# Optimization experiments

Measured on AMD Instinct MI355X. Metric: run time of the kernel, lower is better.

## Reference

```python
import jax, jax.numpy as jnp
import numpy as np

# config constants
B, L, ENC_IN = 8, 512, 7
D_MODEL = 768
EXPAND = 2
D_INNER = D_MODEL * EXPAND          # 1536
DT_RANK = (D_MODEL + 15) // 16      # 48
N_STATE = 16                         # configs.d_ff acts as SSM state size
K_CONV = 4
E_LAYERS = 2
C_OUT = 7
PRED_LEN = 96
EPS = 1e-5


def rmsnorm(x, w):
    return x * jax.lax.rsqrt(jnp.mean(x * x, axis=-1, keepdims=True) + EPS) * w


def silu(x):
    return x * jax.nn.sigmoid(x)


def positional_embedding(l, d):
    pos = np.arange(l, dtype=np.float32)[:, None]
    div = np.exp(np.arange(0, d, 2, dtype=np.float32) * (-np.log(10000.0) / d))
    pe = np.zeros((l, d), dtype=np.float32)
    pe[:, 0::2] = np.sin(pos * div)
    pe[:, 1::2] = np.cos(pos * div)
    return jnp.asarray(pe)


def causal_dwconv(x, w, b):
    # x: [b, d, l], w: [d, 1, k]; torch pads k-1 both sides then slices [:l] == left-pad k-1
    y = jax.lax.conv_general_dilated(
        x, w, window_strides=(1,), padding=[(K_CONV - 1, 0)],
        dimension_numbers=('NCH', 'OIH', 'NCH'), feature_group_count=D_INNER)
    return y + b[None, :, None]


def selective_scan(u, delta, A, Bm, Cm, Dp):
    # u, delta: [b,l,d]; A: [d,n]; Bm, Cm: [b,l,n]; Dp: [d]
    deltaA = jnp.exp(jnp.einsum('bld,dn->bldn', delta, A))          # [b,l,d,n]
    deltaBu = (delta * u)[..., None] * Bm[:, :, None, :]             # [b,l,d,n]

    def step(xc, inp):
        dA, dBu, Ct = inp                                            # [b,d,n],[b,d,n],[b,n]
        xc = dA * xc + dBu
        return xc, jnp.einsum('bdn,bn->bd', xc, Ct)

    b, l, d = u.shape
    x0 = jnp.zeros((b, d, A.shape[1]), u.dtype)
    _, ys = jax.lax.scan(step, x0, (jnp.moveaxis(deltaA, 1, 0),
                                    jnp.moveaxis(deltaBu, 1, 0),
                                    jnp.moveaxis(Cm, 1, 0)))
    y = jnp.moveaxis(ys, 0, 1)                                       # [b,l,d]
    return y + u * Dp


def mamba_block(x, in_w, conv_w, conv_b, xproj_w, dtproj_w, dtproj_b, A_log, Dp, outproj_w):
    xr = x @ in_w.T                                                  # [b,l,2*d_inner]
    xs, res = xr[..., :D_INNER], xr[..., D_INNER:]
    xs = causal_dwconv(jnp.swapaxes(xs, 1, 2), conv_w, conv_b)
    xs = silu(jnp.swapaxes(xs, 1, 2))
    # ssm
    A = -jnp.exp(A_log)
    x_dbl = xs @ xproj_w.T                                           # [b,l,dt_rank+2n]
    delta = x_dbl[..., :DT_RANK]
    Bm = x_dbl[..., DT_RANK:DT_RANK + N_STATE]
    Cm = x_dbl[..., DT_RANK + N_STATE:]
    delta = jax.nn.softplus(delta @ dtproj_w.T + dtproj_b)
    y = selective_scan(xs, delta, A, Bm, Cm, Dp)
    y = y * silu(res)
    return y @ outproj_w.T


def setup_inputs() -> dict:
    key = jax.random.key(0)
    ks = iter(jax.random.split(key, 32))
    s = 0.02
    d = {}
    d['x'] = jax.random.normal(next(ks), (B, L, ENC_IN), jnp.float32)
    d['token_w'] = jax.random.normal(next(ks), (D_MODEL, ENC_IN, 3), jnp.float32) * s
    d['time_w'] = jax.random.normal(next(ks), (D_MODEL, 1), jnp.float32) * s
    d['norm_w'] = jnp.ones((E_LAYERS, D_MODEL), jnp.float32)
    d['in_w'] = jax.random.normal(next(ks), (E_LAYERS, 2 * D_INNER, D_MODEL), jnp.float32) * s
    d['conv_w'] = jax.random.normal(next(ks), (E_LAYERS, D_INNER, 1, K_CONV), jnp.float32) * s
    d['conv_b'] = jnp.zeros((E_LAYERS, D_INNER), jnp.float32)
    d['xproj_w'] = jax.random.normal(next(ks), (E_LAYERS, DT_RANK + 2 * N_STATE, D_INNER), jnp.float32) * s
    d['dtproj_w'] = jax.random.normal(next(ks), (E_LAYERS, D_INNER, DT_RANK), jnp.float32) * s
    d['dtproj_b'] = jnp.zeros((E_LAYERS, D_INNER), jnp.float32)
    A = np.tile(np.arange(1, N_STATE + 1, dtype=np.float32)[None, :], (D_INNER, 1))
    d['A_log'] = jnp.tile(jnp.log(jnp.asarray(A))[None], (E_LAYERS, 1, 1))
    d['Dp'] = jnp.ones((E_LAYERS, D_INNER), jnp.float32)
    d['outproj_w'] = jax.random.normal(next(ks), (E_LAYERS, D_MODEL, D_INNER), jnp.float32) * s
    d['final_norm_w'] = jnp.ones((D_MODEL,), jnp.float32)
    d['out_w'] = jax.random.normal(next(ks), (C_OUT, D_MODEL), jnp.float32) * s
    return d


def reference(x, token_w, time_w, norm_w, in_w, conv_w, conv_b, xproj_w,
              dtproj_w, dtproj_b, A_log, Dp, outproj_w, final_norm_w, out_w):
    # instance normalization (mean/std detached)
    mean_enc = jax.lax.stop_gradient(jnp.mean(x, axis=1, keepdims=True))
    xc = x - mean_enc
    std_enc = jax.lax.stop_gradient(jnp.sqrt(jnp.var(xc, axis=1, keepdims=True) + 1e-5))
    xc = xc / std_enc
    # DataEmbedding: circular conv token emb + sinusoidal pos + timeF linear
    xp = jnp.pad(jnp.swapaxes(xc, 1, 2), ((0, 0), (0, 0), (1, 1)), mode='wrap')
    tok = jax.lax.conv_general_dilated(xp, token_w, (1,), 'VALID',
                                       dimension_numbers=('NCH', 'OIH', 'NCH'))
    tok = jnp.swapaxes(tok, 1, 2)                                    # [b,l,d_model]
    x_mark = (jnp.arange(L, dtype=x.dtype) / L)[None, :, None]       # [1,l,1]
    h = tok + positional_embedding(L, D_MODEL)[None] + x_mark @ time_w.T
    for e in range(E_LAYERS):
        h = mamba_block(rmsnorm(h, norm_w[e]), in_w[e], conv_w[e], conv_b[e],
                        xproj_w[e], dtproj_w[e], dtproj_b[e], A_log[e], Dp[e],
                        outproj_w[e]) + h
    h = rmsnorm(h, final_norm_w)
    out = h @ out_w.T
    out = out * std_enc + mean_enc
    return out[:, -PRED_LEN:, :]
```

## Files before the change

kernel.cpp:

```cpp
#include <hip/hip_runtime.h>
#include <hip/hip_bf16.h>
#include <math.h>

#define BSZ 8
#define LSEQ 512
#define ENC_IN 7
#define D_MODEL 768
#define D_INNER 1536
#define DT_RANK 48
#define N_STATE 16
#define K_CONV 4
#define E_LAYERS 2
#define C_OUT 7
#define PRED_LEN 96
#define EPSV 1e-5f
#define XN 80
#define KSPLIT 4

#define ROWS (BSZ*LSEQ)
#define NC 16
#define CL (LSEQ/NC)
#define NTILE (LSEQ/16)
#define LOG2E 1.44269504088896f

typedef __bf16 bf16x8 __attribute__((ext_vector_type(8)));
typedef float  f32x4  __attribute__((ext_vector_type(4)));

__device__ __forceinline__ float fexp2(float x) {
    float r;
    asm("v_exp_f32 %0, %1" : "=v"(r) : "v"(x));
    return r;
}
__device__ __forceinline__ float softplusf(float v) {
    return fmaxf(v, 0.f) + log1pf(__expf(-fabsf(v)));
}
__device__ __forceinline__ void glds16(const char* g, char* l) {
    __builtin_amdgcn_global_load_lds((const __attribute__((address_space(1))) unsigned int*)g,
                                     (__attribute__((address_space(3))) unsigned int*)l, 16, 0, 0);
}

__device__ __forceinline__ float block_sum(float v, float* tmp) {
    #pragma unroll
    for (int off = 32; off > 0; off >>= 1) v += __shfl_down(v, off);
    int lane = threadIdx.x & 63, wid = threadIdx.x >> 6;
    __syncthreads();
    if (lane == 0) tmp[wid] = v;
    __syncthreads();
    return tmp[0] + tmp[1] + tmp[2] + tmp[3];
}

__global__ __launch_bounds__(256) void cvt_all(const float* __restrict__ in_w,
                                               const float* __restrict__ outw,
                                               const float* __restrict__ xpw,
                                               const float* __restrict__ dtw,
                                               __hip_bfloat16* __restrict__ inw_bf,
                                               __hip_bfloat16* __restrict__ outw_bf,
                                               __hip_bfloat16* __restrict__ xpw_bf,
                                               __hip_bfloat16* __restrict__ dtw_bf) {
    const int N1 = E_LAYERS*2*D_INNER*D_MODEL;
    const int N2 = E_LAYERS*D_MODEL*D_INNER;
    const int N3 = E_LAYERS*XN*D_INNER;
    const int N4 = E_LAYERS*D_INNER*64;
    int i = blockIdx.x*256 + threadIdx.x;
    if (i < N1) {
        inw_bf[i] = __float2bfloat16(in_w[i]);
    } else if (i < N1+N2) {
        int j = i - N1; outw_bf[j] = __float2bfloat16(outw[j]);
    } else if (i < N1+N2+N3) {
        int j = i - N1 - N2; xpw_bf[j] = __float2bfloat16(xpw[j]);
    } else if (i < N1+N2+N3+N4) {
        int j = i - N1 - N2 - N3;
        int r = j >> 6, c = j & 63;
        dtw_bf[j] = __float2bfloat16(c < DT_RANK ? dtw[r*DT_RANK + c] : 0.f);
    }
}

__global__ __launch_bounds__(256) void stats_kernel(const float* __restrict__ x,
                                                    float* __restrict__ mean,
                                                    float* __restrict__ stdv) {
    int bc = blockIdx.x;
    int b = bc / ENC_IN, c = bc % ENC_IN;
    __shared__ float tmp[4];
    float s = 0.f, sq = 0.f;
    for (int l = threadIdx.x; l < LSEQ; l += 256) {
        float v = x[((size_t)(b*LSEQ + l))*ENC_IN + c];
        s += v; sq += v*v;
    }
    s = block_sum(s, tmp);
    sq = block_sum(sq, tmp);
    if (threadIdx.x == 0) {
        float m = s / LSEQ;
        float var = sq / LSEQ - m*m;
        if (var < 0.f) var = 0.f;
        mean[bc] = m;
        stdv[bc] = sqrtf(var + EPSV);
    }
}

__global__ __launch_bounds__(256) void embed_kernel(const float* __restrict__ x,
                                                    const float* __restrict__ token_w,
                                                    const float* __restrict__ time_w,
                                                    const float* __restrict__ mean,
                                                    const float* __restrict__ stdv,
                                                    float* __restrict__ h) {
    int bl = blockIdx.x;
    int b = bl >> 9, l = bl & 511;
    __shared__ float sxc[ENC_IN*3];
    if (threadIdx.x < ENC_IN*3) {
        int c = threadIdx.x / 3, k = threadIdx.x % 3;
        int lk = (l + k - 1) & 511;
        float v = x[((size_t)(b*LSEQ + lk))*ENC_IN + c];
        sxc[threadIdx.x] = (v - mean[b*ENC_IN + c]) / stdv[b*ENC_IN + c];
    }
    __syncthreads();
    #pragma unroll
    for (int i = 0; i < 3; i++) {
        int d = threadIdx.x + i*256;
        float acc = 0.f;
        const float* w = token_w + (size_t)d*21;
        #pragma unroll
        for (int t = 0; t < 21; t++) acc += sxc[t] * w[t];
        int d2 = d & ~1;
        float div = __expf((float)d2 * (-9.210340371976184f / (float)D_MODEL));
        float ang = (float)l * div;
        float pe = (d & 1) ? cosf(ang) : sinf(ang);
        float tm = ((float)l / (float)LSEQ) * time_w[d];
        h[(size_t)bl*D_MODEL + d] = acc + pe + tm;
    }
}

__global__ __launch_bounds__(256) void rmsnorm_bf16(const float* __restrict__ h,
                                                    const float* __restrict__ w,
                                                    __hip_bfloat16* __restrict__ xn) {
    size_t base = (size_t)blockIdx.x * D_MODEL;
    __shared__ float tmp[4];
    int tid = threadIdx.x;
    f32x4 v = {0.f,0.f,0.f,0.f};
    if (tid < 192) v = *(const f32x4*)(h + base + tid*4);
    float ss = v[0]*v[0] + v[1]*v[1] + v[2]*v[2] + v[3]*v[3];
    ss = block_sum(ss, tmp);
    float inv = rsqrtf(ss / (float)D_MODEL + EPSV);
    if (tid < 192) {
        f32x4 wv = *(const f32x4*)(w + tid*4);
        __hip_bfloat16 o4[4];
        #pragma unroll
        for (int j = 0; j < 4; j++) o4[j] = __float2bfloat16(v[j]*inv*wv[j]);
        *(uint2*)(xn + base + tid*4) = *(uint2*)o4;
    }
}

__global__ __launch_bounds__(256, 2) void gemm_inproj(const __hip_bfloat16* __restrict__ A,
                                                      const __hip_bfloat16* __restrict__ Bw,
                                                      __hip_bfloat16* __restrict__ Cxs,
                                                      __hip_bfloat16* __restrict__ Cg) {
    __shared__ __align__(16) __hip_bfloat16 As[3][128*32];
    __shared__ __align__(16) __hip_bfloat16 Bs[3][256*32];
    const int K = D_MODEL;
    const int NK = K/32;
    int tid = threadIdx.x, lane = tid & 63, w = tid >> 6;
    int gx = gridDim.x;
    int nwg = gx * gridDim.y;
    int orig = blockIdx.y*gx + blockIdx.x;
    int swz = (orig & 7)*(nwg >> 3) + (orig >> 3);
    int m0 = (swz / gx) * 128, n0 = (swz % gx) * 256;
    int wr = w >> 1, wc = w & 1;
    int kq = lane >> 4, rr = lane & 15;

    f32x4 acc[4][8];
    #pragma unroll
    for (int i = 0; i < 4; i++)
        #pragma unroll
        for (int j = 0; j < 8; j++) acc[i][j] = (f32x4){0.f,0.f,0.f,0.f};

    const char* Ab = (const char*)A;
    const char* Bb = (const char*)Bw;
    char* AsB = (char*)As;
    char* BsB = (char*)Bs;

    int cA0 = tid, cA1 = tid + 256;
    int rA0 = cA0 >> 2, qA0 = (cA0 & 3) ^ ((rA0 >> 1) & 3);
    int rA1 = cA1 >> 2, qA1 = (cA1 & 3) ^ ((rA1 >> 1) & 3);
    int sw = (kq ^ ((rr >> 1) & 3)) * 16;

    auto stage = [&](int buf, int kt) {
        int k0 = kt*32;
        glds16(Ab + ((size_t)(m0+rA0)*K + k0 + qA0*8)*2, AsB + buf*8192 + cA0*16);
        glds16(Ab + ((size_t)(m0+rA1)*K + k0 + qA1*8)*2, AsB + buf*8192 + cA1*16);
        #pragma unroll
        for (int j = 0; j < 4; j++) {
            int idx = j*256 + tid;
            int r = idx >> 2, q = (idx & 3) ^ ((r >> 1) & 3);
            glds16(Bb + ((size_t)(n0+r)*K + k0 + q*8)*2, BsB + buf*16384 + idx*16);
        }
    };

    stage(0, 0);
    stage(1, 1);

    for (int k = 0; k < NK; k++) {
        int cur = k % 3;
        __builtin_amdgcn_s_barrier();
        if (k + 2 < NK) stage((k + 2) % 3, k + 2);
        if (k + 2 < NK)      asm volatile("s_waitcnt vmcnt(12)" ::: "memory");
        else if (k + 1 < NK) asm volatile("s_waitcnt vmcnt(6)" ::: "memory");
        else                 asm volatile("s_waitcnt vmcnt(0)" ::: "memory");
        __builtin_amdgcn_s_barrier();
        bf16x8 af[4], bfr[8];
        #pragma unroll
        for (int mi = 0; mi < 4; mi++) af[mi]  = *(const bf16x8*)(AsB + cur*8192  + (wr*64 + mi*16 + rr)*64 + sw);
        #pragma unroll
        for (int ni = 0; ni < 8; ni++) bfr[ni] = *(const bf16x8*)(BsB + cur*16384 + (wc*128 + ni*16 + rr)*64 + sw);
        __builtin_amdgcn_s_setprio(1);
        #pragma unroll
        for (int mi = 0; mi < 4; mi++)
            #pragma unroll
            for (int ni = 0; ni < 8; ni++)
                acc[mi][ni] = __builtin_amdgcn_mfma_f32_16x16x32_bf16(af[mi], bfr[ni], acc[mi][ni], 0, 0, 0);
        __builtin_amdgcn_s_setprio(0);
    }

    #pragma unroll
    for (int mi = 0; mi < 4; mi++) {
        #pragma unroll
        for (int ni = 0; ni < 8; ni++) {
            int row0 = m0 + wr*64 + mi*16;
            int col  = n0 + wc*128 + ni*16 + rr;
            if (col >= D_INNER) {
                __hip_bfloat16 g4[4];
                #pragma unroll
                for (int r = 0; r < 4; r++) {
                    float v = acc[mi][ni][r];
                    g4[r] = __float2bfloat16(v / (1.f + __expf(-v)));
                }
                int cd = col - D_INNER;
                *(uint2*)&Cg[((size_t)(row0 >> 4)*D_INNER + cd)*16 + kq*4] = *(uint2*)g4;
            } else {
                #pragma unroll
                for (int r = 0; r < 4; r++) {
                    int row = row0 + kq*4 + r;
                    Cxs[(size_t)row*D_INNER + col] = __float2bfloat16(acc[mi][ni][r]);
                }
            }
        }
    }
}

__global__ __launch_bounds__(256) void gemm_dtproj(const float* __restrict__ P,
                                                   const __hip_bfloat16* __restrict__ Bw,
                                                   const float* __restrict__ bias,
                                                   float* __restrict__ xdbl,
                                                   __hip_bfloat16* __restrict__ delta) {
    __shared__ __align__(16) __hip_bfloat16 As[128*64];
    __shared__ __align__(16) __hip_bfloat16 Bs[128*64];
    const int K = 64;
    int tid = threadIdx.x, lane = tid & 63, w = tid >> 6;
    int gx = gridDim.x;
    int nwg = gx * gridDim.y;
    int orig = blockIdx.y*gx + blockIdx.x;
    int swz = (orig & 7)*(nwg >> 3) + (orig >> 3);
    int m0 = (swz / gx) * 128, n0 = (swz % gx) * 128;
    int wr = w >> 1, wc = w & 1;
    int kq = lane >> 4, rr = lane & 15;

    f32x4 acc[4][4];
    #pragma unroll
    for (int i = 0; i < 4; i++)
        #pragma unroll
        for (int j = 0; j < 4; j++) acc[i][j] = (f32x4){0.f,0.f,0.f,0.f};

    const char* Bb = (const char*)Bw;
    char* AsB = (char*)As;
    char* BsB = (char*)Bs;

    #pragma unroll
    for (int c = 0; c < 4; c++) {
        int idx = c*256 + tid;
        int r = idx >> 3, q = idx & 7;
        int qs = q ^ (r & 7);
        glds16(Bb + ((size_t)(n0+r)*K + qs*8)*2, BsB + idx*16);
    }

    const size_t RX = (size_t)ROWS*XN;
    #pragma unroll
    for (int it = 0; it < 2; it++) {
        int idx = it*1024 + tid;
        if (idx < 128*10) {
            int row = idx / 10, ch = idx % 10;
            const float* p0 = P + (size_t)(m0+row)*XN + ch*8;
            f32x4 a0 = *(const f32x4*)(p0)      + *(const f32x4*)(p0+RX)
                     + *(const f32x4*)(p0+2*RX) + *(const f32x4*)(p0+3*RX);
            f32x4 a1 = *(const f32x4*)(p0+4)        + *(const f32x4*)(p0+RX+4)
                     + *(const f32x4*)(p0+2*RX+4)   + *(const f32x4*)(p0+3*RX+4);
            if (n0 == 0) {
                float* xd = xdbl + (size_t)(m0+row)*XN + ch*8;
                *(f32x4*)(xd)   = a0;
                *(f32x4*)(xd+4) = a1;
            }
            if (ch < 8) {
                bf16x8 hv;
                if (ch < 6) {
                    #pragma unroll
                    for (int j = 0; j < 4; j++) { hv[j] = (__bf16)a0[j]; hv[4+j] = (__bf16)a1[j]; }
                } else {
                    bf16x8 z = {}; hv = z;
                }
                *(bf16x8*)(AsB + row*128 + ((ch ^ (row & 7))*16)) = hv;
            }
        }
    }
    __syncthreads();

    #pragma unroll
    for (int kh = 0; kh < 2; kh++) {
        int ch = ((kh*4 + kq) ^ (rr & 7)) * 16;
        bf16x8 af[4], bfr[4];
        #pragma unroll
        for (int mi = 0; mi < 4; mi++) af[mi]  = *(const bf16x8*)(AsB + (wr*64 + mi*16 + rr)*128 + ch);
        #pragma unroll
        for (int ni = 0; ni < 4; ni++) bfr[ni] = *(const bf16x8*)(BsB + (wc*64 + ni*16 + rr)*128 + ch);
        #pragma unroll
        for (int mi = 0; mi < 4; mi++)
            #pragma unroll
            for (int ni = 0; ni < 4; ni++)
                acc[mi][ni] = __builtin_amdgcn_mfma_f32_16x16x32_bf16(af[mi], bfr[ni], acc[mi][ni], 0, 0, 0);
    }

    #pragma unroll
    for (int mi = 0; mi < 4; mi++) {
        #pragma unroll
        for (int ni = 0; ni < 4; ni++) {
            int row0 = m0 + wr*64 + mi*16;
            int col  = n0 + wc*64 + ni*16 + rr;
            __hip_bfloat16 d4[4];
            #pragma unroll
            for (int r = 0; r < 4; r++) {
                float v = acc[mi][ni][r] + bias[col];
                d4[r] = __float2bfloat16(softplusf(v));
            }
            *(uint2*)&delta[((size_t)(row0 >> 4)*D_INNER + col)*16 + kq*4] = *(uint2*)d4;
        }
    }
}

__global__ __launch_bounds__(256) void gemm_outproj(const __hip_bfloat16* __restrict__ A,
                                                    const __hip_bfloat16* __restrict__ Bw,
                                                    float* __restrict__ C) {
    __shared__ __align__(16) __hip_bfloat16 As[3][128*32];
    __shared__ __align__(16) __hip_bfloat16 Bs[3][128*32];
    int tid = threadIdx.x, lane = tid & 63, w = tid >> 6;
    int gx = gridDim.x;
    int nwg = gx * gridDim.y;
    int orig = blockIdx.y*gx + blockIdx.x;
    int swz = (orig & 7)*(nwg >> 3) + (orig >> 3);
    int m0 = (swz / gx) * 128, n0 = (swz % gx) * 128;
    int wr = w >> 1, wc = w & 1;
    int kq = lane >> 4, rr = lane & 15;
    const int K = D_INNER;
    const int kbase = blockIdx.z * (D_INNER/2);
    const int NK = (D_INNER/2)/32;

    f32x4 acc[4][4];
    #pragma unroll
    for (int i = 0; i < 4; i++)
        #pragma unroll
        for (int j = 0; j < 4; j++) acc[i][j] = (f32x4){0.f,0.f,0.f,0.f};

    const char* Ab = (const char*)A;
    const char* Bb = (const char*)Bw;
    char* AsB = (char*)As;
    char* BsB = (char*)Bs;

    int c0 = tid, c1 = tid + 256;
    int r0 = c0 >> 2, q0 = (c0 & 3) ^ ((r0 >> 1) & 3);
    int r1 = c1 >> 2, q1 = (c1 & 3) ^ ((r1 >> 1) & 3);
    int sw = (kq ^ ((rr >> 1) & 3)) * 16;

    auto stage = [&](int buf, int kt) {
        int k0 = kbase + kt*32;
        glds16(Ab + ((size_t)(m0+r0)*K + k0 + q0*8)*2, AsB + buf*8192 + c0*16);
        glds16(Ab + ((size_t)(m0+r1)*K + k0 + q1*8)*2, AsB + buf*8192 + c1*16);
        glds16(Bb + ((size_t)(n0+r0)*K + k0 + q0*8)*2, BsB + buf*8192 + c0*16);
        glds16(Bb + ((size_t)(n0+r1)*K + k0 + q1*8)*2, BsB + buf*8192 + c1*16);
    };

    stage(0, 0);
    stage(1, 1);

    for (int k = 0; k < NK; k++) {
        int cur = k % 3;
        __builtin_amdgcn_s_barrier();
        if (k + 2 < NK) stage((k + 2) % 3, k + 2);
        if (k + 2 < NK)      asm volatile("s_waitcnt vmcnt(8)" ::: "memory");
        else if (k + 1 < NK) asm volatile("s_waitcnt vmcnt(4)" ::: "memory");
        else                 asm volatile("s_waitcnt vmcnt(0)" ::: "memory");
        __builtin_amdgcn_s_barrier();
        bf16x8 af[4], bfr[4];
        #pragma unroll
        for (int mi = 0; mi < 4; mi++) af[mi]  = *(const bf16x8*)(AsB + cur*8192 + (wr*64 + mi*16 + rr)*64 + sw);
        #pragma unroll
        for (int ni = 0; ni < 4; ni++) bfr[ni] = *(const bf16x8*)(BsB + cur*8192 + (wc*64 + ni*16 + rr)*64 + sw);
        __builtin_amdgcn_s_setprio(1);
        #pragma unroll
        for (int mi = 0; mi < 4; mi++)
            #pragma unroll
            for (int ni = 0; ni < 4; ni++)
                acc[mi][ni] = __builtin_amdgcn_mfma_f32_16x16x32_bf16(af[mi], bfr[ni], acc[mi][ni], 0, 0, 0);
        __builtin_amdgcn_s_setprio(0);
    }

    #pragma unroll
    for (int mi = 0; mi < 4; mi++) {
        #pragma unroll
        for (int ni = 0; ni < 4; ni++) {
            #pragma unroll
            for (int r = 0; r < 4; r++) {
                int row = m0 + wr*64 + mi*16 + kq*4 + r;
                int col = n0 + wc*64 + ni*16 + rr;
                atomicAdd(&C[(size_t)row*D_MODEL + col], acc[mi][ni][r]);
            }
        }
    }
}

__global__ __launch_bounds__(256) void gemm_xproj(const __hip_bfloat16* __restrict__ A,
                                                  const __hip_bfloat16* __restrict__ W,
                                                  float* __restrict__ P) {
    __shared__ __align__(16) __hip_bfloat16 As[3][64*64];
    __shared__ __align__(16) __hip_bfloat16 Bs[3][96*64];
    int tid = threadIdx.x, lane = tid & 63, w = tid >> 6;
    int m0 = blockIdx.x * 64;
    int k0 = blockIdx.y * (D_INNER / KSPLIT);
    int kq = lane >> 4, rr = lane & 15;
    const int NK = (D_INNER/KSPLIT)/64;
    f32x4 acc[5];
    #pragma unroll
    for (int i = 0; i < 5; i++) acc[i] = (f32x4){0.f,0.f,0.f,0.f};
    const char* Ab = (const char*)A;
    const char* Wb = (const char*)W;
    char* AsB = (char*)As;
    char* BsB = (char*)Bs;

    auto stage = [&](int buf, int it) {
        int kk = k0 + it*64;
        #pragma unroll
        for (int cA = 0; cA < 2; cA++) {
            int idx = cA*256 + tid;
            int r = idx >> 3, q = (idx & 7) ^ (r & 7);
            glds16(Ab + ((size_t)(m0+r)*D_INNER + kk + q*8)*2, AsB + buf*8192 + idx*16);
        }
        #pragma unroll
        for (int cB = 0; cB < 3; cB++) {
            int idx = cB*256 + tid;
            int r = idx >> 3, q = (idx & 7) ^ (r & 7);
            int rs = r < XN ? r : XN-1;
            glds16(Wb + ((size_t)rs*D_INNER + kk + q*8)*2, BsB + buf*12288 + idx*16);
        }
    };

    stage(0, 0);
    stage(1, 1);

    for (int it = 0; it < NK; it++) {
        int cur = it % 3;
        __builtin_amdgcn_s_barrier();
        if (it + 2 < NK) stage((it + 2) % 3, it + 2);
        if (it + 2 < NK)      asm volatile("s_waitcnt vmcnt(10)" ::: "memory");
        else if (it + 1 < NK) asm volatile("s_waitcnt vmcnt(5)" ::: "memory");
        else                  asm volatile("s_waitcnt vmcnt(0)" ::: "memory");
        __builtin_amdgcn_s_barrier();
        #pragma unroll
        for (int kh = 0; kh < 2; kh++) {
            bf16x8 a = *(const bf16x8*)(AsB + cur*8192 + (w*16 + rr)*128 + (((kh*4 + kq) ^ (rr & 7)))*16);
            #pragma unroll
            for (int ni = 0; ni < 5; ni++) {
                bf16x8 b = *(const bf16x8*)(BsB + cur*12288 + (ni*16 + rr)*128 + (((kh*4 + kq) ^ (rr & 7)))*16);
                acc[ni] = __builtin_amdgcn_mfma_f32_16x16x32_bf16(a, b, acc[ni], 0, 0, 0);
            }
        }
    }
    float* Cp = P + (size_t)blockIdx.y * ROWS * XN;
    #pragma unroll
    for (int ni = 0; ni < 5; ni++)
        #pragma unroll
        for (int r = 0; r < 4; r++) {
            int row = m0 + w*16 + kq*4 + r;
            int col = ni*16 + rr;
            Cp[(size_t)row*XN + col] = acc[ni][r];
        }
}

__global__ __launch_bounds__(256) void dwconv_silu(const __hip_bfloat16* __restrict__ xs,
                                                   const float* __restrict__ cw,
                                                   const float* __restrict__ cb,
                                                   __hip_bfloat16* __restrict__ u_bf) {
    int idx = blockIdx.x*256 + threadIdx.x;
    int dg = idx % (D_INNER/8);
    int t  = idx / (D_INNER/8);
    if (t >= ROWS) return;
    int d0 = dg*8;
    int l = t & 511, b = t >> 9;
    bf16x8 rows[K_CONV];
    #pragma unroll
    for (int k = 0; k < K_CONV; k++) {
        int ll = l - (K_CONV-1) + k;
        if (ll >= 0) rows[k] = *(const bf16x8*)(xs + ((size_t)(b*LSEQ + ll))*D_INNER + d0);
        else { bf16x8 z = {}; rows[k] = z; }
    }
    bf16x8 outv;
    #pragma unroll
    for (int j = 0; j < 8; j++) {
        int d = d0 + j;
        const float4 w4 = *(const float4*)(cw + d*K_CONV);
        float acc = cb[d]
                  + (float)rows[0][j]*w4.x + (float)rows[1][j]*w4.y
                  + (float)rows[2][j]*w4.z + (float)rows[3][j]*w4.w;
        float v = acc / (1.f + __expf(-acc));
        outv[j] = (__bf16)v;
    }
    *(bf16x8*)(u_bf + (size_t)t*D_INNER + d0) = outv;
}

__global__ __launch_bounds__(256) void scan_p1(const __hip_bfloat16* __restrict__ u,
                                               const __hip_bfloat16* __restrict__ delta_blk,
                                               const float* __restrict__ xdbl,
                                               const float* __restrict__ A_log,
                                               float* __restrict__ xfin,
                                               float* __restrict__ sumdlt) {
    int d = blockIdx.x*256 + threadIdx.x;
    int c = blockIdx.y, b = blockIdx.z;
    int l0 = c*CL;
    const float* al = A_log + d*N_STATE;
    bool fast = true;
    #pragma unroll
    for (int n = 0; n < N_STATE; n++)
        fast = fast && (fabsf(__expf(al[n]) - (float)(n+1)) < 1e-3f);
    float xs[N_STATE];
    #pragma unroll
    for (int n = 0; n < N_STATE; n++) xs[n] = 0.f;
    const __hip_bfloat16* pu = u + (size_t)(b*LSEQ + l0)*D_INNER + d;
    const float* pB = xdbl + (size_t)(b*LSEQ + l0)*XN + DT_RANK;
    float sd = 0.f;
    if (fast) {
        #pragma unroll
        for (int tt = 0; tt < 2; tt++) {
            const __hip_bfloat16* db = delta_blk + ((size_t)(b*NTILE + (l0>>4) + tt)*D_INNER + d)*16;
            bf16x8 d0 = *(const bf16x8*)db;
            bf16x8 d1 = *(const bf16x8*)(db + 8);
            #pragma unroll
            for (int i = 0; i < 16; i++) {
                float dlt = (float)(i < 8 ? d0[i] : d1[i-8]);
                float uu = __bfloat162float(*pu); pu += D_INNER;
                float du = dlt*uu;
                sd += dlt;
                float e1 = fexp2(-dlt*LOG2E);
                float e = e1;
                xs[0] = e*xs[0] + du*pB[0];
                #pragma unroll
                for (int n = 1; n < N_STATE; n++) {
                    e *= e1;
                    xs[n] = e*xs[n] + du*pB[n];
                }
                pB += XN;
            }
        }
    } else {
        #pragma unroll
        for (int tt = 0; tt < 2; tt++) {
            const __hip_bfloat16* db = delta_blk + ((size_t)(b*NTILE + (l0>>4) + tt)*D_INNER + d)*16;
            bf16x8 d0 = *(const bf16x8*)db;
            bf16x8 d1 = *(const bf16x8*)(db + 8);
            #pragma unroll
            for (int i = 0; i < 16; i++) {
                float dlt = (float)(i < 8 ? d0[i] : d1[i-8]);
                float uu = __bfloat162float(*pu); pu += D_INNER;
                float du = dlt*uu;
                sd += dlt;
                #pragma unroll
                for (int n = 0; n < N_STATE; n++) {
                    float A2n = -__expf(al[n]) * LOG2E;
                    xs[n] = fexp2(dlt*A2n)*xs[n] + du*pB[n];
                }
                pB += XN;
            }
        }
    }
    float* px = xfin + (size_t)((b*NC + c)*N_STATE)*D_INNER + d;
    #pragma unroll
    for (int n = 0; n < N_STATE; n++) px[n*D_INNER] = xs[n];
    sumdlt[(size_t)(b*NC + c)*D_INNER + d] = sd;
}

__global__ __launch_bounds__(256) void scan_p2(float* __restrict__ xfin,
                                               const float* __restrict__ sumdlt,
                                               const float* __restrict__ A_log) {
    int idx = blockIdx.x*256 + threadIdx.x;
    int d = idx % D_INNER;
    int r = idx / D_INNER;
    int n = r & 15;
    int b = r >> 4;
    float A2 = -__expf(A_log[d*N_STATE + n]) * LOG2E;
    float cr = 0.f;
    for (int c = 1; c < NC; c++) {
        size_t jp = (size_t)(b*NC + c - 1);
        float xf = xfin[(jp*N_STATE + n)*D_INNER + d];
        float s  = sumdlt[jp*D_INNER + d];
        cr = fexp2(A2 * s) * cr + xf;
        xfin[(jp*N_STATE + n)*D_INNER + d] = cr;
    }
}

__global__ __launch_bounds__(256) void scan_p3(const __hip_bfloat16* __restrict__ u,
                                               const __hip_bfloat16* __restrict__ delta_blk,
                                               const __hip_bfloat16* __restrict__ gres,
                                               const float* __restrict__ xdbl,
                                               const float* __restrict__ A_log,
                                               const float* __restrict__ Dp,
                                               const float* __restrict__ carry,
                                               __hip_bfloat16* __restrict__ ygate) {
    int d = blockIdx.x*256 + threadIdx.x;
    int c = blockIdx.y, b = blockIdx.z;
    int l0 = c*CL;
    const float* al = A_log + d*N_STATE;
    bool fast = true;
    #pragma unroll
    for (int n = 0; n < N_STATE; n++)
        fast = fast && (fabsf(__expf(al[n]) - (float)(n+1)) < 1e-3f);
    float xs[N_STATE];
    if (c == 0) {
        #pragma unroll
        for (int n = 0; n < N_STATE; n++) xs[n] = 0.f;
    } else {
        const float* pc = carry + (size_t)((b*NC + c - 1)*N_STATE)*D_INNER + d;
        #pragma unroll
        for (int n = 0; n < N_STATE; n++) xs[n] = pc[n*D_INNER];
    }
    float Dv = Dp[d];
    const __hip_bfloat16* pu = u + (size_t)(b*LSEQ + l0)*D_INNER + d;
    const float* pB = xdbl + (size_t)(b*LSEQ + l0)*XN + DT_RANK;
    __hip_bfloat16* py = ygate + (size_t)(b*LSEQ + l0)*D_INNER + d;
    if (fast) {
        #pragma unroll
        for (int tt = 0; tt < 2; tt++) {
            size_t tb = (size_t)(b*NTILE + (l0>>4) + tt)*D_INNER + d;
            const __hip_bfloat16* db = delta_blk + tb*16;
            bf16x8 d0 = *(const bf16x8*)db;
            bf16x8 d1 = *(const bf16x8*)(db + 8);
            const __hip_bfloat16* gb = gres + tb*16;
            bf16x8 g0 = *(const bf16x8*)gb;
            bf16x8 g1 = *(const bf16x8*)(gb + 8);
            #pragma unroll
            for (int i = 0; i < 16; i++) {
                float dlt = (float)(i < 8 ? d0[i] : d1[i-8]);
                float gr  = (float)(i < 8 ? g0[i] : g1[i-8]);
                float uu = __bfloat162float(*pu); pu += D_INNER;
                float du = dlt*uu;
                float e1 = fexp2(-dlt*LOG2E);
                float e = e1;
                float acc;
                xs[0] = e*xs[0] + du*pB[0];
                acc = xs[0]*pB[N_STATE + 0];
                #pragma unroll
                for (int n = 1; n < N_STATE; n++) {
                    e *= e1;
                    xs[n] = e*xs[n] + du*pB[n];
                    acc += xs[n]*pB[N_STATE + n];
                }
                pB += XN;
                float y = acc + uu*Dv;
                *py = __float2bfloat16(y * gr); py += D_INNER;
            }
        }
    } else {
        #pragma unroll
        for (int tt = 0; tt < 2; tt++) {
            size_t tb = (size_t)(b*NTILE + (l0>>4) + tt)*D_INNER + d;
            const __hip_bfloat16* db = delta_blk + tb*16;
            bf16x8 d0 = *(const bf16x8*)db;
            bf16x8 d1 = *(const bf16x8*)(db + 8);
            const __hip_bfloat16* gb = gres + tb*16;
            bf16x8 g0 = *(const bf16x8*)gb;
            bf16x8 g1 = *(const bf16x8*)(gb + 8);
            #pragma unroll
            for (int i = 0; i < 16; i++) {
                float dlt = (float)(i < 8 ? d0[i] : d1[i-8]);
                float gr  = (float)(i < 8 ? g0[i] : g1[i-8]);
                float uu = __bfloat162float(*pu); pu += D_INNER;
                float du = dlt*uu;
                float acc = 0.f;
                #pragma unroll
                for (int n = 0; n < N_STATE; n++) {
                    float A2n = -__expf(al[n]) * LOG2E;
                    xs[n] = fexp2(dlt*A2n)*xs[n] + du*pB[n];
                    acc += xs[n]*pB[N_STATE + n];
                }
                pB += XN;
                float y = acc + uu*Dv;
                *py = __float2bfloat16(y * gr); py += D_INNER;
            }
        }
    }
}

__global__ __launch_bounds__(256) void final_kernel(const float* __restrict__ h,
                                                    const float* __restrict__ fnw,
                                                    const float* __restrict__ out_w,
                                                    const float* __restrict__ mean,
                                                    const float* __restrict__ stdv,
                                                    float* __restrict__ out) {
    int bid = blockIdx.x;
    int b = bid / PRED_LEN, lo = bid % PRED_LEN;
    int l = LSEQ - PRED_LEN + lo;
    const float* row = h + ((size_t)(b*LSEQ + l))*D_MODEL;
    __shared__ float tmp[4];
    float ss = 0.f;
    for (int k = threadIdx.x; k < D_MODEL; k += 256) { float v = row[k]; ss += v*v; }
    ss = block_sum(ss, tmp);
    float inv = rsqrtf(ss / (float)D_MODEL + EPSV);
    float acc[C_OUT] = {};
    for (int k = threadIdx.x; k < D_MODEL; k += 256) {
        float hn = row[k]*fnw[k];
        #pragma unroll
        for (int c = 0; c < C_OUT; c++) acc[c] += hn*out_w[c*D_MODEL + k];
    }
    #pragma unroll
    for (int c = 0; c < C_OUT; c++) {
        float s = block_sum(acc[c], tmp);
        if (threadIdx.x == 0)
            out[((size_t)(b*PRED_LEN + lo))*C_OUT + c] = s*inv*stdv[b*ENC_IN + c] + mean[b*ENC_IN + c];
    }
}

extern "C" void kernel_launch(void* const* d_in, const int* in_sizes, int n_in,
                              void* d_out, int out_size, void* d_ws, size_t ws_size,
                              hipStream_t stream) {
    const float* x        = (const float*)d_in[0];
    const float* token_w  = (const float*)d_in[1];
    const float* time_w   = (const float*)d_in[2];
    const float* norm_w   = (const float*)d_in[3];
    const float* in_w     = (const float*)d_in[4];
    const float* conv_w   = (const float*)d_in[5];
    const float* conv_b   = (const float*)d_in[6];
    const float* xproj_w  = (const float*)d_in[7];
    const float* dtproj_w = (const float*)d_in[8];
    const float* dtproj_b = (const float*)d_in[9];
    const float* A_log    = (const float*)d_in[10];
    const float* Dp       = (const float*)d_in[11];
    const float* outproj_w= (const float*)d_in[12];
    const float* final_nw = (const float*)d_in[13];
    const float* out_w    = (const float*)d_in[14];
    float* out = (float*)d_out;

    float* ws   = (float*)d_ws;
    float* mean = ws;
    float* stdv = ws + 64;
    float* h    = ws + 128;
    float* xdbl = h    + (size_t)ROWS*D_MODEL;
    float* sumd = xdbl + (size_t)ROWS*XN;
    float* xfin = sumd + (size_t)BSZ*NC*D_INNER;
    float* pout = xfin + (size_t)BSZ*NC*D_INNER*N_STATE;
    float* fend = pout + (size_t)KSPLIT*ROWS*XN;
    __hip_bfloat16* xn_bf  = (__hip_bfloat16*)fend;
    __hip_bfloat16* xs_bf  = xn_bf + (size_t)ROWS*D_MODEL;
    __hip_bfloat16* u_bf   = xs_bf + (size_t)ROWS*D_INNER;
    __hip_bfloat16* gres   = u_bf  + (size_t)ROWS*D_INNER;
    __hip_bfloat16* ygate  = gres  + (size_t)ROWS*D_INNER;
    __hip_bfloat16* delta  = ygate + (size_t)ROWS*D_INNER;
    __hip_bfloat16* inw_bf = delta + (size_t)ROWS*D_INNER;
    __hip_bfloat16* outw_bf= inw_bf + (size_t)E_LAYERS*2*D_INNER*D_MODEL;
    __hip_bfloat16* xpw_bf = outw_bf+ (size_t)E_LAYERS*D_MODEL*D_INNER;
    __hip_bfloat16* dtw_bf = xpw_bf + (size_t)E_LAYERS*XN*D_INNER;

    {
        const int NT = E_LAYERS*2*D_INNER*D_MODEL + E_LAYERS*D_MODEL*D_INNER
                     + E_LAYERS*XN*D_INNER + E_LAYERS*D_INNER*64;
        cvt_all<<<(NT+255)/256, 256, 0, stream>>>(in_w, outproj_w, xproj_w, dtproj_w,
                                                  inw_bf, outw_bf, xpw_bf, dtw_bf);
    }

    stats_kernel<<<BSZ*ENC_IN, 256, 0, stream>>>(x, mean, stdv);
    embed_kernel<<<ROWS, 256, 0, stream>>>(x, token_w, time_w, mean, stdv, h);

    for (int e = 0; e < E_LAYERS; e++) {
        rmsnorm_bf16<<<ROWS, 256, 0, stream>>>(h, norm_w + e*D_MODEL, xn_bf);
        gemm_inproj<<<dim3(2*D_INNER/256, ROWS/128), 256, 0, stream>>>(
            xn_bf, inw_bf + (size_t)e*2*D_INNER*D_MODEL, xs_bf, gres);
        dwconv_silu<<<(ROWS*(D_INNER/8) + 255)/256, 256, 0, stream>>>(
            xs_bf, conv_w + (size_t)e*D_INNER*K_CONV, conv_b + e*D_INNER, u_bf);
        gemm_xproj<<<dim3(ROWS/64, KSPLIT), 256, 0, stream>>>(
            u_bf, xpw_bf + (size_t)e*XN*D_INNER, pout);
        gemm_dtproj<<<dim3(D_INNER/128, ROWS/128), 256, 0, stream>>>(
            pout, dtw_bf + (size_t)e*D_INNER*64, dtproj_b + e*D_INNER, xdbl, delta);
        const float* Alog_e = A_log + (size_t)e*D_INNER*N_STATE;
        scan_p1<<<dim3(D_INNER/256, NC, BSZ), 256, 0, stream>>>(
            u_bf, delta, xdbl, Alog_e, xfin, sumd);
        scan_p2<<<(BSZ*D_INNER*N_STATE)/256, 256, 0, stream>>>(
            xfin, sumd, Alog_e);
        scan_p3<<<dim3(D_INNER/256, NC, BSZ), 256, 0, stream>>>(
            u_bf, delta, gres, xdbl, Alog_e, Dp + (size_t)e*D_INNER, xfin, ygate);
        gemm_outproj<<<dim3(D_MODEL/128, ROWS/128, 2), 256, 0, stream>>>(
            ygate, outw_bf + (size_t)e*D_MODEL*D_INNER, h);
    }

    final_kernel<<<BSZ*PRED_LEN, 256, 0, stream>>>(h, final_nw, out_w, mean, stdv, out);
}
```

Baseline: 401.3 us.

## Double-buffer inproj GEMM and drop split-K atomics in outproj with narrower tiles

The in-projection GEMM goes from a three-stage to a two-stage LDS pipeline with an extra barrier per iteration, which cuts shared memory and lifts the explicit two-blocks-per-CU launch bound. The out-projection GEMM drops its two-way split-K with atomicAdd. It now uses 128x64 tiles over the full K and does a plain read-add-store residual update, so the grid keeps a similar block count without atomic traffic. In exchange the inproj loses prefetch depth, and each outproj block runs twice as many K iterations.

Result: no change. 401.8 us (+0.1%).

```diff
diff --git a/kernel.cpp b/kernel.cpp
--- a/kernel.cpp
+++ b/kernel.cpp
@@ -149,12 +149,12 @@
     }
 }
 
-__global__ __launch_bounds__(256, 2) void gemm_inproj(const __hip_bfloat16* __restrict__ A,
-                                                      const __hip_bfloat16* __restrict__ Bw,
-                                                      __hip_bfloat16* __restrict__ Cxs,
-                                                      __hip_bfloat16* __restrict__ Cg) {
-    __shared__ __align__(16) __hip_bfloat16 As[3][128*32];
-    __shared__ __align__(16) __hip_bfloat16 Bs[3][256*32];
+__global__ __launch_bounds__(256) void gemm_inproj(const __hip_bfloat16* __restrict__ A,
+                                                   const __hip_bfloat16* __restrict__ Bw,
+                                                   __hip_bfloat16* __restrict__ Cxs,
+                                                   __hip_bfloat16* __restrict__ Cg) {
+    __shared__ __align__(16) __hip_bfloat16 As[2][128*32];
+    __shared__ __align__(16) __hip_bfloat16 Bs[2][256*32];
     const int K = D_MODEL;
     const int NK = K/32;
     int tid = threadIdx.x, lane = tid & 63, w = tid >> 6;
@@ -195,15 +195,15 @@
     };
 
     stage(0, 0);
-    stage(1, 1);
 
     for (int k = 0; k < NK; k++) {
-        int cur = k % 3;
-        __builtin_amdgcn_s_barrier();
-        if (k + 2 < NK) stage((k + 2) % 3, k + 2);
-        if (k + 2 < NK)      asm volatile("s_waitcnt vmcnt(12)" ::: "memory");
-        else if (k + 1 < NK) asm volatile("s_waitcnt vmcnt(6)" ::: "memory");
-        else                 asm volatile("s_waitcnt vmcnt(0)" ::: "memory");
+        int cur = k & 1;
+        if (k + 1 < NK) {
+            stage(cur ^ 1, k + 1);
+            asm volatile("s_waitcnt vmcnt(6)" ::: "memory");
+        } else {
+            asm volatile("s_waitcnt vmcnt(0)" ::: "memory");
+        }
         __builtin_amdgcn_s_barrier();
         bf16x8 af[4], bfr[8];
         #pragma unroll
@@ -217,6 +217,7 @@
             for (int ni = 0; ni < 8; ni++)
                 acc[mi][ni] = __builtin_amdgcn_mfma_f32_16x16x32_bf16(af[mi], bfr[ni], acc[mi][ni], 0, 0, 0);
         __builtin_amdgcn_s_setprio(0);
+        __builtin_amdgcn_s_barrier();
     }
 
     #pragma unroll
@@ -346,41 +347,40 @@
                                                     const __hip_bfloat16* __restrict__ Bw,
                                                     float* __restrict__ C) {
     __shared__ __align__(16) __hip_bfloat16 As[3][128*32];
-    __shared__ __align__(16) __hip_bfloat16 Bs[3][128*32];
+    __shared__ __align__(16) __hip_bfloat16 Bs[3][64*32];
     int tid = threadIdx.x, lane = tid & 63, w = tid >> 6;
     int gx = gridDim.x;
     int nwg = gx * gridDim.y;
     int orig = blockIdx.y*gx + blockIdx.x;
     int swz = (orig & 7)*(nwg >> 3) + (orig >> 3);
-    int m0 = (swz / gx) * 128, n0 = (swz % gx) * 128;
+    int m0 = (swz / gx) * 128, n0 = (swz % gx) * 64;
     int wr = w >> 1, wc = w & 1;
     int kq = lane >> 4, rr = lane & 15;
     const int K = D_INNER;
-    const int kbase = blockIdx.z * (D_INNER/2);
-    const int NK = (D_INNER/2)/32;
-
-    f32x4 acc[4][4];
+    const int NK = K/32;
+
+    f32x4 acc[4][2];
     #pragma unroll
     for (int i = 0; i < 4; i++)
         #pragma unroll
-        for (int j = 0; j < 4; j++) acc[i][j] = (f32x4){0.f,0.f,0.f,0.f};
+        for (int j = 0; j < 2; j++) acc[i][j] = (f32x4){0.f,0.f,0.f,0.f};
 
     const char* Ab = (const char*)A;
     const char* Bb = (const char*)Bw;
     char* AsB = (char*)As;
     char* BsB = (char*)Bs;
 
-    int c0 = tid, c1 = tid + 256;
-    int r0 = c0 >> 2, q0 = (c0 & 3) ^ ((r0 >> 1) & 3);
-    int r1 = c1 >> 2, q1 = (c1 & 3) ^ ((r1 >> 1) & 3);
+    int cA0 = tid, cA1 = tid + 256;
+    int rA0 = cA0 >> 2, qA0 = (cA0 & 3) ^ ((rA0 >> 1) & 3);
+    int rA1 = cA1 >> 2, qA1 = (cA1 & 3) ^ ((rA1 >> 1) & 3);
+    int rB = tid >> 2,  qB  = (tid & 3) ^ ((rB >> 1) & 3);
     int sw = (kq ^ ((rr >> 1) & 3)) * 16;
 
     auto stage = [&](int buf, int kt) {
-        int k0 = kbase + kt*32;
-        glds16(Ab + ((size_t)(m0+r0)*K + k0 + q0*8)*2, AsB + buf*8192 + c0*16);
-        glds16(Ab + ((size_t)(m0+r1)*K + k0 + q1*8)*2, AsB + buf*8192 + c1*16);
-        glds16(Bb + ((size_t)(n0+r0)*K + k0 + q0*8)*2, BsB + buf*8192 + c0*16);
-        glds16(Bb + ((size_t)(n0+r1)*K + k0 + q1*8)*2, BsB + buf*8192 + c1*16);
+        int k0 = kt*32;
+        glds16(Ab + ((size_t)(m0+rA0)*K + k0 + qA0*8)*2, AsB + buf*8192 + cA0*16);
+        glds16(Ab + ((size_t)(m0+rA1)*K + k0 + qA1*8)*2, AsB + buf*8192 + cA1*16);
+        glds16(Bb + ((size_t)(n0+rB)*K + k0 + qB*8)*2,  BsB + buf*4096 + tid*16);
     };
 
     stage(0, 0);
@@ -390,20 +390,20 @@
         int cur = k % 3;
         __builtin_amdgcn_s_barrier();
         if (k + 2 < NK) stage((k + 2) % 3, k + 2);
-        if (k + 2 < NK)      asm volatile("s_waitcnt vmcnt(8)" ::: "memory");
-        else if (k + 1 < NK) asm volatile("s_waitcnt vmcnt(4)" ::: "memory");
+        if (k + 2 < NK)      asm volatile("s_waitcnt vmcnt(6)" ::: "memory");
+        else if (k + 1 < NK) asm volatile("s_waitcnt vmcnt(3)" ::: "memory");
         else                 asm volatile("s_waitcnt vmcnt(0)" ::: "memory");
         __builtin_amdgcn_s_barrier();
-        bf16x8 af[4], bfr[4];
+        bf16x8 af[4], bfr[2];
         #pragma unroll
         for (int mi = 0; mi < 4; mi++) af[mi]  = *(const bf16x8*)(AsB + cur*8192 + (wr*64 + mi*16 + rr)*64 + sw);
         #pragma unroll
-        for (int ni = 0; ni < 4; ni++) bfr[ni] = *(const bf16x8*)(BsB + cur*8192 + (wc*64 + ni*16 + rr)*64 + sw);
+        for (int ni = 0; ni < 2; ni++) bfr[ni] = *(const bf16x8*)(BsB + cur*4096 + (wc*32 + ni*16 + rr)*64 + sw);
         __builtin_amdgcn_s_setprio(1);
         #pragma unroll
         for (int mi = 0; mi < 4; mi++)
             #pragma unroll
-            for (int ni = 0; ni < 4; ni++)
+            for (int ni = 0; ni < 2; ni++)
                 acc[mi][ni] = __builtin_amdgcn_mfma_f32_16x16x32_bf16(af[mi], bfr[ni], acc[mi][ni], 0, 0, 0);
         __builtin_amdgcn_s_setprio(0);
     }
@@ -411,12 +411,13 @@
     #pragma unroll
     for (int mi = 0; mi < 4; mi++) {
         #pragma unroll
-        for (int ni = 0; ni < 4; ni++) {
+        for (int ni = 0; ni < 2; ni++) {
             #pragma unroll
             for (int r = 0; r < 4; r++) {
                 int row = m0 + wr*64 + mi*16 + kq*4 + r;
-                int col = n0 + wc*64 + ni*16 + rr;
-                atomicAdd(&C[(size_t)row*D_MODEL + col], acc[mi][ni][r]);
+                int col = n0 + wc*32 + ni*16 + rr;
+                size_t o = (size_t)row*D_MODEL + col;
+                C[o] = acc[mi][ni][r] + C[o];
             }
         }
     }
@@ -797,7 +798,7 @@
             xfin, sumd, Alog_e);
         scan_p3<<<dim3(D_INNER/256, NC, BSZ), 256, 0, stream>>>(
             u_bf, delta, gres, xdbl, Alog_e, Dp + (size_t)e*D_INNER, xfin, ygate);
-        gemm_outproj<<<dim3(D_MODEL/128, ROWS/128, 2), 256, 0, stream>>>(
+        gemm_outproj<<<dim3(D_MODEL/64, ROWS/128), 256, 0, stream>>>(
             ygate, outw_bf + (size_t)e*D_MODEL*D_INNER, h);
     }
 
```
